# Kernel optimization log

Hardware: AMD Instinct MI355X
Metric: run time of the kernel (lower is better)

The kernel has to match this reference:

```python
import jax, jax.numpy as jnp
import numpy as np

DIM = 3072
NUM_HEADS = 24
HEAD_DIM = DIM // NUM_HEADS  # 128
EPS = 1e-6


def rms_norm(x, scale):
    # x: (..., D); torch F.rms_norm over last dim
    var = jnp.mean(jnp.square(x), axis=-1, keepdims=True)
    return x * jax.lax.rsqrt(var + EPS) * scale


def apply_rope(xq, xk, freqs_cis):
    # xq, xk: (B, H, L, D); freqs_cis: (1, 1, L, D//2, 2, 2)
    B, H, L, D = xq.shape
    xq_ = xq.astype(jnp.float32).reshape(B, H, L, D // 2, 1, 2)
    xk_ = xk.astype(jnp.float32).reshape(B, H, L, D // 2, 1, 2)
    # (1,1,L,D/2,2) * (B,H,L,D/2,1) broadcast -> (B,H,L,D/2,2)
    xq_out = freqs_cis[..., 0] * xq_[..., 0] + freqs_cis[..., 1] * xq_[..., 1]
    xk_out = freqs_cis[..., 0] * xk_[..., 0] + freqs_cis[..., 1] * xk_[..., 1]
    return xq_out.reshape(B, H, L, D).astype(xq.dtype), xk_out.reshape(B, H, L, D).astype(xk.dtype)


def setup_inputs() -> dict:
    key = jax.random.key(0)
    ks = jax.random.split(key, 7)
    B, L = 1, 2048
    x = jax.random.normal(ks[0], (B, L, DIM), dtype=jnp.float32)
    pe = jax.random.normal(ks[1], (1, 1, L, HEAD_DIM // 2, 2, 2), dtype=jnp.float32)
    # parameters (torch nn.Linear layout: weight is (out, in))
    s = 1.0 / np.sqrt(DIM)
    w_qkv = jax.random.uniform(ks[2], (3 * DIM, DIM), minval=-s, maxval=s, dtype=jnp.float32)
    w_proj = jax.random.uniform(ks[3], (DIM, DIM), minval=-s, maxval=s, dtype=jnp.float32)
    b_proj = jax.random.uniform(ks[4], (DIM,), minval=-s, maxval=s, dtype=jnp.float32)
    q_scale = jnp.ones((HEAD_DIM,), dtype=jnp.float32)
    k_scale = jnp.ones((HEAD_DIM,), dtype=jnp.float32)
    return {"x": x, "pe": pe, "w_qkv": w_qkv, "w_proj": w_proj,
            "b_proj": b_proj, "q_scale": q_scale, "k_scale": k_scale}


def reference(x, pe, w_qkv, w_proj, b_proj, q_scale, k_scale):
    B, L, _ = x.shape
    qkv = x @ w_qkv.T  # (B, L, 3*DIM)
    qkv = qkv.reshape(B, L, 3, NUM_HEADS, HEAD_DIM)
    qkv = jnp.transpose(qkv, (2, 0, 3, 1, 4))  # (3, B, H, L, D)
    q, k, v = qkv[0], qkv[1], qkv[2]
    # QKNorm (RMSNorm over head_dim)
    q = rms_norm(q, q_scale)
    k = rms_norm(k, k_scale)
    # RoPE
    q, k = apply_rope(q, k, pe)
    # SDPA: softmax(q k^T / sqrt(D)) v, non-causal
    scores = jnp.einsum("bhqd,bhkd->bhqk", q, k) / np.sqrt(HEAD_DIM).astype(np.float32)
    attn = jax.nn.softmax(scores, axis=-1)
    out = jnp.einsum("bhqk,bhkd->bhqd", attn, v)  # (B, H, L, D)
    out = jnp.transpose(out, (0, 2, 1, 3)).reshape(B, L, DIM)  # B L (H D)
    return out @ w_proj.T + b_proj
```

## Files before the change

### kernel.cpp

```cpp
#include <hip/hip_runtime.h>
#include <hip/hip_bf16.h>

typedef _Float16 f16;
typedef _Float16 f16x2 __attribute__((ext_vector_type(2)));
typedef _Float16 f16x4 __attribute__((ext_vector_type(4)));
typedef _Float16 f16x8 __attribute__((ext_vector_type(8)));
typedef float f32x4 __attribute__((ext_vector_type(4)));

#define L_SEQ 2048
#define DIM 3072
#define NHEAD 24
#define HDIM 128

__device__ __forceinline__ void gll16(const f16* g, f16* l) {
    __builtin_amdgcn_global_load_lds((const __attribute__((address_space(1))) void*)g,
                                     (__attribute__((address_space(3))) void*)l, 16, 0, 0);
}

__global__ __launch_bounds__(256) void f32_to_f16_kernel(const float* __restrict__ s,
                                                         f16* __restrict__ d, int n4) {
    int i = blockIdx.x * blockDim.x + threadIdx.x;
    int stride = gridDim.x * blockDim.x;
    for (; i < n4; i += stride) {
        float4 v = reinterpret_cast<const float4*>(s)[i];
        f16x4 o = {(f16)v.x, (f16)v.y, (f16)v.z, (f16)v.w};
        reinterpret_cast<f16x4*>(d)[i] = o;
    }
}


#define GEMM_BODY(T, VM, DO_STAGE)                                                      \
    {                                                                                   \
        asm volatile("s_waitcnt vmcnt(" #VM ")" ::: "memory");                          \
        __builtin_amdgcn_s_barrier();                                                   \
        __builtin_amdgcn_sched_barrier(0);                                              \
        const int slot_ = (T) & 3;                                                      \
        f16x8 af[4], bf[4];                                                             \
        _Pragma("unroll") for (int i = 0; i < 4; i++)                                   \
            af[i] = *reinterpret_cast<const f16x8*>(                                    \
                &As[slot_][(wr + i * 16 + laneM) * 32 + fc16]);                         \
        _Pragma("unroll") for (int j = 0; j < 4; j++)                                   \
            bf[j] = *reinterpret_cast<const f16x8*>(                                    \
                &Bs[slot_][(wc + j * 16 + laneM) * 32 + fc16]);                         \
        if (DO_STAGE) {                                                                 \
            const int t3 = (T) + 3;                                                     \
            const int s3 = t3 & 3;                                                      \
            gll16(Asrc0 + t3 * 32, &As[s3][dstoff]);                                    \
            gll16(Asrc1 + t3 * 32, &As[s3][4096 + dstoff]);                             \
            gll16(Bsrc + t3 * 32, &Bs[s3][dstoff]);                                     \
        }                                                                               \
        __builtin_amdgcn_s_setprio(1);                                                  \
        _Pragma("unroll") for (int i = 0; i < 4; i++)                                   \
            _Pragma("unroll") for (int j = 0; j < 4; j++)                               \
                acc[i][j] =                                                             \
                    __builtin_amdgcn_mfma_f32_16x16x32_f16(af[i], bf[j], acc[i][j],     \
                                                           0, 0, 0);                    \
        __builtin_amdgcn_s_setprio(0);                                                  \
    }

template <int MODE>
__global__ __launch_bounds__(512) void rg_gemm(const f16* __restrict__ A,
                                               const f16* __restrict__ B,
                                               f16* __restrict__ Cf16,
                                               float* __restrict__ Cf32,
                                               const float* __restrict__ bias,
                                               int M, int N, int K) {
    __shared__ f16 As[4][256 * 32];
    __shared__ f16 Bs[4][128 * 32];
    const int tid = threadIdx.x;
    const int wid = tid >> 6;
    const int lane = tid & 63;
    const int grp = lane >> 4;
    const int laneM = lane & 15;
    const int m0 = blockIdx.y * 256;
    const int n0 = blockIdx.x * 128;
    const int wr = (wid >> 1) * 64;
    const int wc = (wid & 1) * 64;
    const int NT = K >> 5;
    const int fc16 = (grp ^ ((laneM >> 1) & 3)) * 8;

    const int srow = tid >> 2;
    const int scol = (((tid & 3) ^ ((tid >> 3) & 3)) << 3);
    const f16* Asrc0 = A + (size_t)(m0 + srow) * K + scol;
    const f16* Asrc1 = A + (size_t)(m0 + 128 + srow) * K + scol;
    const f16* Bsrc = B + (size_t)(n0 + srow) * K + scol;
    const int dstoff = wid * 512;

    const f32x4 vzero = {0.f, 0.f, 0.f, 0.f};
    f32x4 acc[4][4];
#pragma unroll
    for (int i = 0; i < 4; i++)
#pragma unroll
        for (int j = 0; j < 4; j++) acc[i][j] = vzero;

#pragma unroll
    for (int t = 0; t < 3; t++) {
        const int s = t & 3;
        gll16(Asrc0 + t * 32, &As[s][dstoff]);
        gll16(Asrc1 + t * 32, &As[s][4096 + dstoff]);
        gll16(Bsrc + t * 32, &Bs[s][dstoff]);
    }

    int t = 0;
    for (; t < NT - 3; ++t) GEMM_BODY(t, 6, true);
    GEMM_BODY(t, 6, false); ++t;
    GEMM_BODY(t, 3, false); ++t;
    GEMM_BODY(t, 0, false);

#pragma unroll
    for (int i = 0; i < 4; i++)
#pragma unroll
        for (int j = 0; j < 4; j++)
#pragma unroll
            for (int r = 0; r < 4; r++) {
                int row = m0 + wr + i * 16 + grp * 4 + r;
                int col = n0 + wc + j * 16 + laneM;
                float v = acc[i][j][r];
                if (MODE == 0) {
                    Cf16[(size_t)row * N + col] = (f16)v;
                } else {
                    Cf32[(size_t)row * N + col] = v + bias[col];
                }
            }
}

__global__ __launch_bounds__(64) void fuse_qk_kernel(const f16* __restrict__ qkv,
                                                     const float* __restrict__ pe,
                                                     const float* __restrict__ qs,
                                                     const float* __restrict__ ks,
                                                     f16* __restrict__ qb,
                                                     f16* __restrict__ kb) {
    const int l = blockIdx.x;
    const int h = blockIdx.y;
    const int i = threadIdx.x;
    const f16* row = qkv + (size_t)l * (3 * DIM) + h * HDIM;
    f16x2 qp = *reinterpret_cast<const f16x2*>(row + 2 * i);
    f16x2 kp = *reinterpret_cast<const f16x2*>(row + DIM + 2 * i);
    float q0 = (float)qp[0], q1 = (float)qp[1];
    float k0 = (float)kp[0], k1 = (float)kp[1];
    float sq = q0 * q0 + q1 * q1;
    float sk = k0 * k0 + k1 * k1;
#pragma unroll
    for (int off = 1; off < 64; off <<= 1) {
        sq += __shfl_xor(sq, off);
        sk += __shfl_xor(sk, off);
    }
    const float SCALE = 0.08838834764831845f;
    float rq = rsqrtf(sq * (1.0f / 128.0f) + 1e-6f) * SCALE;
    float rk = rsqrtf(sk * (1.0f / 128.0f) + 1e-6f);
    float4 w = *reinterpret_cast<const float4*>(pe + ((size_t)l * 64 + i) * 4);
    float qa = q0 * rq * qs[2 * i];
    float qbv = q1 * rq * qs[2 * i + 1];
    float ka = k0 * rk * ks[2 * i];
    float kbv = k1 * rk * ks[2 * i + 1];
    f16x2 qo = {(f16)(w.x * qa + w.y * qbv), (f16)(w.z * qa + w.w * qbv)};
    f16x2 ko = {(f16)(w.x * ka + w.y * kbv), (f16)(w.z * ka + w.w * kbv)};
    *reinterpret_cast<f16x2*>(qb + ((size_t)h * L_SEQ + l) * HDIM + 2 * i) = qo;
    *reinterpret_cast<f16x2*>(kb + ((size_t)h * L_SEQ + l) * HDIM + 2 * i) = ko;
}

__global__ __launch_bounds__(256) void transpose_v_kernel(const f16* __restrict__ qkv,
                                                          f16* __restrict__ vT) {
    __shared__ f16 tile[32][33];
    const int tx = threadIdx.x & 31;
    const int ty = threadIdx.x >> 5;
    const int c0 = blockIdx.x * 32;
    const int r0 = blockIdx.y * 32;
#pragma unroll
    for (int j = 0; j < 4; j++)
        tile[ty + j * 8][tx] = qkv[(size_t)(r0 + ty + j * 8) * (3 * DIM) + 2 * DIM + c0 + tx];
    __syncthreads();
#pragma unroll
    for (int j = 0; j < 4; j++)
        vT[(size_t)(c0 + ty + j * 8) * L_SEQ + r0 + tx] = tile[tx][ty + j * 8];
}

#define KVBLK 64
#define NSTEP (L_SEQ / KVBLK)

__device__ __forceinline__ void stage_kv(const f16* __restrict__ Kh,
                                         const f16* __restrict__ Vh,
                                         int k0, f16* Kt, f16* Vt, int tid) {
    const int wid = tid >> 6;
    const int krow = tid >> 4;
    const int kcl = (tid & 15) ^ (krow & 7);
    const int vrow = tid >> 3;
    const int vcl = (tid & 7) ^ (vrow & 7);
#pragma unroll
    for (int i = 0; i < 4; i++)
        gll16(Kh + (size_t)(k0 + i * 16 + krow) * HDIM + kcl * 8, Kt + i * 2048 + wid * 512);
#pragma unroll
    for (int i = 0; i < 4; i++)
        gll16(Vh + (size_t)(i * 32 + vrow) * L_SEQ + k0 + vcl * 8, Vt + i * 2048 + wid * 512);
}

__global__ __launch_bounds__(256, 2) void attn_kernel(const f16* __restrict__ qb,
                                                      const f16* __restrict__ kb,
                                                      const f16* __restrict__ vT,
                                                      f16* __restrict__ attnb) {
    __shared__ f16 Kt[2][64 * 128];
    __shared__ f16 Vt[2][128 * 64];
    __shared__ f16 Pl[4][16 * 72];
    const int tid = threadIdx.x;
    const int wid = tid >> 6;
    const int lane = tid & 63;
    const int grp = lane >> 4;
    const int laneM = lane & 15;
    const int h = blockIdx.y;
    const int q0 = blockIdx.x * 64 + wid * 16;
    const f16* Qh = qb + (size_t)h * L_SEQ * HDIM;
    const f16* Kh = kb + (size_t)h * L_SEQ * HDIM;
    const f16* Vh = vT + (size_t)h * HDIM * L_SEQ;

    f16x8 qf[4];
#pragma unroll
    for (int c = 0; c < 4; c++)
        qf[c] = *reinterpret_cast<const f16x8*>(Qh + (size_t)(q0 + laneM) * HDIM + c * 32 + grp * 8);

    const f32x4 vzero = {0.f, 0.f, 0.f, 0.f};
    f32x4 O[8];
#pragma unroll
    for (int f = 0; f < 8; f++) O[f] = vzero;
    float m = -3.0e38f;
    float lsum = 0.f;
    f16* Prow = &Pl[wid][laneM * 72];
    const int swz = laneM & 7;

    stage_kv(Kh, Vh, 0, Kt[0], Vt[0], tid);

    for (int step = 0; step < NSTEP; ++step) {
        const int cur = step & 1;
        __syncthreads();
        if (step + 1 < NSTEP)
            stage_kv(Kh, Vh, (step + 1) * KVBLK, Kt[cur ^ 1], Vt[cur ^ 1], tid);
        const f16* Kc = Kt[cur];
        const f16* Vc = Vt[cur];

        f32x4 s[4];
#pragma unroll
        for (int cc = 0; cc < 4; cc++) s[cc] = vzero;
#pragma unroll
        for (int cc = 0; cc < 4; cc++) {
            f16x8 kf[4];
#pragma unroll
            for (int c = 0; c < 4; c++)
                kf[c] = *reinterpret_cast<const f16x8*>(
                    &Kc[(cc * 16 + laneM) * 128 + (((c * 4 + grp) ^ swz) * 8)]);
#pragma unroll
            for (int c = 0; c < 4; c++)
                s[cc] = __builtin_amdgcn_mfma_f32_16x16x32_f16(kf[c], qf[c], s[cc], 0, 0, 0);
        }

        float pmax = s[0][0];
#pragma unroll
        for (int cc = 0; cc < 4; cc++)
#pragma unroll
            for (int r = 0; r < 4; r++) pmax = fmaxf(pmax, s[cc][r]);
        if (!__all(pmax <= m + 8.0f)) {
            float pm = fmaxf(pmax, __shfl_xor(pmax, 16));
            pm = fmaxf(pm, __shfl_xor(pm, 32));
            float mnew = fmaxf(m, pm);
            float alpha = __expf(m - mnew);
            m = mnew;
            lsum *= alpha;
            float af[4];
#pragma unroll
            for (int r = 0; r < 4; r++) af[r] = __shfl(alpha, grp * 4 + r);
#pragma unroll
            for (int f = 0; f < 8; f++)
#pragma unroll
                for (int r = 0; r < 4; r++) O[f][r] *= af[r];
        }
        float ps = 0.f;
#pragma unroll
        for (int cc = 0; cc < 4; cc++) {
            f16x4 pk;
#pragma unroll
            for (int r = 0; r < 4; r++) {
                float p = __expf(s[cc][r] - m);
                ps += p;
                pk[r] = (f16)p;
            }
            *reinterpret_cast<f16x4*>(Prow + cc * 16 + grp * 4) = pk;
        }
        ps += __shfl_xor(ps, 16);
        ps += __shfl_xor(ps, 32);
        lsum += ps;

#pragma unroll
        for (int z = 0; z < 2; z++) {
            f16x8 pa = *reinterpret_cast<const f16x8*>(Prow + z * 32 + grp * 8);
#pragma unroll
            for (int f = 0; f < 8; f++) {
                f16x8 vf = *reinterpret_cast<const f16x8*>(
                    &Vc[(f * 16 + laneM) * 64 + (((z * 4 + grp) ^ swz) * 8)]);
                O[f] = __builtin_amdgcn_mfma_f32_16x16x32_f16(pa, vf, O[f], 0, 0, 0);
            }
        }
    }

    float li = 1.0f / lsum;
    float lf[4];
#pragma unroll
    for (int r = 0; r < 4; r++) lf[r] = __shfl(li, grp * 4 + r);
#pragma unroll
    for (int f = 0; f < 8; f++)
#pragma unroll
        for (int r = 0; r < 4; r++) {
            int row = q0 + grp * 4 + r;
            attnb[(size_t)row * DIM + h * HDIM + f * 16 + laneM] = (f16)(O[f][r] * lf[r]);
        }
}

extern "C" void kernel_launch(void* const* d_in, const int* in_sizes, int n_in,
                              void* d_out, int out_size, void* d_ws, size_t ws_size,
                              hipStream_t stream) {
    const float* x = (const float*)d_in[0];
    const float* pe = (const float*)d_in[1];
    const float* w_qkv = (const float*)d_in[2];
    const float* w_proj = (const float*)d_in[3];
    const float* b_proj = (const float*)d_in[4];
    const float* q_scale = (const float*)d_in[5];
    const float* k_scale = (const float*)d_in[6];
    float* out = (float*)d_out;

    char* ws = (char*)d_ws;
    f16* xb     = (f16*)(ws + 0);
    f16* wqkvb  = (f16*)(ws + 12582912);
    f16* wprojb = (f16*)(ws + 69206016);
    f16* qkvb   = (f16*)(ws + 88080384);
    f16* qbuf   = (f16*)(ws + 125829120);
    f16* kbuf   = (f16*)(ws + 138412032);
    f16* vT     = (f16*)(ws + 150994944);
    f16* attnb  = (f16*)(ws + 163577856);
    if (ws_size < 176160768) return;

    f32_to_f16_kernel<<<1024, 256, 0, stream>>>(x, xb, (2048 * 3072) / 4);
    f32_to_f16_kernel<<<2048, 256, 0, stream>>>(w_qkv, wqkvb, (9216 * 3072) / 4);
    f32_to_f16_kernel<<<1024, 256, 0, stream>>>(w_proj, wprojb, (3072 * 3072) / 4);

    rg_gemm<0><<<dim3(72, 8), 512, 0, stream>>>(xb, wqkvb, qkvb, nullptr, nullptr,
                                                2048, 9216, 3072);
    fuse_qk_kernel<<<dim3(2048, 24), 64, 0, stream>>>(qkvb, pe, q_scale, k_scale, qbuf, kbuf);
    transpose_v_kernel<<<dim3(96, 64), 256, 0, stream>>>(qkvb, vT);
    attn_kernel<<<dim3(32, 24), 256, 0, stream>>>(qbuf, kbuf, vT, attnb);
    rg_gemm<1><<<dim3(24, 8), 512, 0, stream>>>(attnb, wprojb, nullptr, out, b_proj,
                                                2048, 3072, 3072);
}
```

Before: 397.5 us.

## Shrink GEMM LDS ring to three stages and remap workgroups for L2 locality

Cuts the shared-memory staging ring from four slots to three, prefetching two tiles ahead instead of three, and adds a min-blocks hint to launch_bounds. The aim is to lower LDS use per block so more workgroups can be resident per CU. Workgroup IDs are also remapped in groups of eight so that neighbouring blocks share A/B tiles in cache. The shallower prefetch depth leaves less room to hide memory latency, and modulo-3 slot indexing is slightly costlier than a mask.

New measurement: 392.4 us. About the same (-1.3%).

```diff
diff --git a/kernel.cpp b/kernel.cpp
--- a/kernel.cpp
+++ b/kernel.cpp
@@ -34,7 +34,7 @@
         asm volatile("s_waitcnt vmcnt(" #VM ")" ::: "memory");                          \
         __builtin_amdgcn_s_barrier();                                                   \
         __builtin_amdgcn_sched_barrier(0);                                              \
-        const int slot_ = (T) & 3;                                                      \
+        const int slot_ = (T) % 3;                                                      \
         f16x8 af[4], bf[4];                                                             \
         _Pragma("unroll") for (int i = 0; i < 4; i++)                                   \
             af[i] = *reinterpret_cast<const f16x8*>(                                    \
@@ -43,11 +43,11 @@
             bf[j] = *reinterpret_cast<const f16x8*>(                                    \
                 &Bs[slot_][(wc + j * 16 + laneM) * 32 + fc16]);                         \
         if (DO_STAGE) {                                                                 \
-            const int t3 = (T) + 3;                                                     \
-            const int s3 = t3 & 3;                                                      \
-            gll16(Asrc0 + t3 * 32, &As[s3][dstoff]);                                    \
-            gll16(Asrc1 + t3 * 32, &As[s3][4096 + dstoff]);                             \
-            gll16(Bsrc + t3 * 32, &Bs[s3][dstoff]);                                     \
+            const int t2 = (T) + 2;                                                     \
+            const int s2 = t2 % 3;                                                      \
+            gll16(Asrc0 + t2 * 32, &As[s2][dstoff]);                                    \
+            gll16(Asrc1 + t2 * 32, &As[s2][4096 + dstoff]);                             \
+            gll16(Bsrc + t2 * 32, &Bs[s2][dstoff]);                                     \
         }                                                                               \
         __builtin_amdgcn_s_setprio(1);                                                  \
         _Pragma("unroll") for (int i = 0; i < 4; i++)                                   \
@@ -59,21 +59,28 @@
     }
 
 template <int MODE>
-__global__ __launch_bounds__(512) void rg_gemm(const f16* __restrict__ A,
-                                               const f16* __restrict__ B,
-                                               f16* __restrict__ Cf16,
-                                               float* __restrict__ Cf32,
-                                               const float* __restrict__ bias,
-                                               int M, int N, int K) {
-    __shared__ f16 As[4][256 * 32];
-    __shared__ f16 Bs[4][128 * 32];
+__global__ __launch_bounds__(512, 4) void rg_gemm(const f16* __restrict__ A,
+                                                  const f16* __restrict__ B,
+                                                  f16* __restrict__ Cf16,
+                                                  float* __restrict__ Cf32,
+                                                  const float* __restrict__ bias,
+                                                  int M, int N, int K) {
+    __shared__ f16 As[3][256 * 32];
+    __shared__ f16 Bs[3][128 * 32];
     const int tid = threadIdx.x;
     const int wid = tid >> 6;
     const int lane = tid & 63;
     const int grp = lane >> 4;
     const int laneM = lane & 15;
-    const int m0 = blockIdx.y * 256;
-    const int n0 = blockIdx.x * 128;
+
+    const int nwg = gridDim.x * gridDim.y;
+    const int orig = blockIdx.y * gridDim.x + blockIdx.x;
+    const int wgid = (orig & 7) * (nwg >> 3) + (orig >> 3);
+    const int bx = wgid % gridDim.x;
+    const int by = wgid / gridDim.x;
+    const int m0 = by * 256;
+    const int n0 = bx * 128;
+
     const int wr = (wid >> 1) * 64;
     const int wc = (wid & 1) * 64;
     const int NT = K >> 5;
@@ -94,16 +101,14 @@
         for (int j = 0; j < 4; j++) acc[i][j] = vzero;
 
 #pragma unroll
-    for (int t = 0; t < 3; t++) {
-        const int s = t & 3;
-        gll16(Asrc0 + t * 32, &As[s][dstoff]);
-        gll16(Asrc1 + t * 32, &As[s][4096 + dstoff]);
-        gll16(Bsrc + t * 32, &Bs[s][dstoff]);
+    for (int t = 0; t < 2; t++) {
+        gll16(Asrc0 + t * 32, &As[t][dstoff]);
+        gll16(Asrc1 + t * 32, &As[t][4096 + dstoff]);
+        gll16(Bsrc + t * 32, &Bs[t][dstoff]);
     }
 
     int t = 0;
-    for (; t < NT - 3; ++t) GEMM_BODY(t, 6, true);
-    GEMM_BODY(t, 6, false); ++t;
+    for (; t < NT - 2; ++t) GEMM_BODY(t, 3, true);
     GEMM_BODY(t, 3, false); ++t;
     GEMM_BODY(t, 0, false);
 
```
